# Kernel optimization log

Measured on AMD Instinct MI355X. Metric: run time of the kernel, lower is better.

The kernel has to match this reference:

```python
import jax, jax.numpy as jnp
import numpy as np

N_EXAMPLES = 10  # hardcoded repeat_interleave(10) in the source

def setup_inputs() -> dict:
    key = jax.random.key(0)
    k1, k2, k3, k4 = jax.random.split(key, 4)
    B, L, S, H = 8, 256, 512, 1024
    return {
        "output": jax.random.normal(k1, (B * N_EXAMPLES, L, H), dtype=jnp.float32),
        "context0": jax.random.normal(k2, (B * N_EXAMPLES, L, H), dtype=jnp.float32),
        "context1": jax.random.normal(k3, (B, S, H), dtype=jnp.float32),
        "mask": jnp.zeros((B * N_EXAMPLES, L), dtype=bool),
        "W_out": jax.random.normal(k4, (H, 3 * H), dtype=jnp.float32) * 0.02,
        "b_out": jnp.zeros((H,), dtype=jnp.float32),
    }

def reference(output, context0, context1, mask, W_out, b_out):
    # output, context0: [B*10, L, H]; context1: [B, S, H]
    # NOTE: in the torch source, `attn.data.masked_fill(mask, -inf)` is NOT
    # in-place and its result is discarded, so the mask has no effect on the
    # math. We reproduce that faithfully: `mask` is unused.
    del mask
    set_ctx = jnp.repeat(context1, N_EXAMPLES, axis=0)  # [B*10, S, H]
    # example-attention branch: bmm -> softmax -> bmm
    ex_attn = jax.nn.softmax(jnp.einsum('bld,bsd->bls', output, context0), axis=-1)  # [B*10, L, L]
    # set-attention branch: bmm -> softmax -> bmm
    set_attn = jax.nn.softmax(jnp.einsum('bld,bsd->bls', output, set_ctx), axis=-1)  # [B*10, L, S]
    ex_c = jnp.einsum('bls,bsd->bld', ex_attn, context0)   # [B*10, L, H]
    set_c = jnp.einsum('bls,bsd->bld', set_attn, set_ctx)  # [B*10, L, H]
    all_info = jnp.concatenate([output, ex_c, set_c], axis=-1)  # [B*10, L, 3H]
    out = jnp.tanh(jnp.einsum('blk,hk->blh', all_info, W_out) + b_out)  # [B*10, L, H]
    return (out, ex_attn, set_attn)
```

## Files before the change

kernel.cpp:

```cpp
#include <hip/hip_runtime.h>
#include <stdint.h>
#include <math.h>

typedef unsigned short u16;
typedef __attribute__((ext_vector_type(8))) short short8;
typedef __attribute__((ext_vector_type(4))) float floatx4;

__device__ __forceinline__ u16 f32_to_bf16(float f) {
    union { float f; uint32_t u; } v; v.f = f;
    uint32_t r = v.u + 0x7FFF + ((v.u >> 16) & 1);
    return (u16)(r >> 16);
}
__device__ __forceinline__ float bf16_to_f32(u16 h) {
    union { uint32_t u; float f; } v; v.u = ((uint32_t)h) << 16; return v.f;
}

__device__ __forceinline__ void gl_lds16(const u16* g, u16* l) {
    __builtin_amdgcn_global_load_lds(
        (const __attribute__((address_space(1))) void*)g,
        (__attribute__((address_space(3))) void*)l, 16, 0, 0);
}


__global__ void split_kernel(const float4* __restrict__ x, ushort4* __restrict__ hi,
                             ushort4* __restrict__ lo, long n4) {
    long i = (long)blockIdx.x * blockDim.x + threadIdx.x;
    if (i >= n4) return;
    float4 v = x[i];
    ushort4 h, l;
    h.x = f32_to_bf16(v.x); l.x = f32_to_bf16(v.x - bf16_to_f32(h.x));
    h.y = f32_to_bf16(v.y); l.y = f32_to_bf16(v.y - bf16_to_f32(h.y));
    h.z = f32_to_bf16(v.z); l.z = f32_to_bf16(v.z - bf16_to_f32(h.z));
    h.w = f32_to_bf16(v.w); l.w = f32_to_bf16(v.w - bf16_to_f32(h.w));
    hi[i] = h; lo[i] = l;
}

__global__ void conv_kernel(const float4* __restrict__ x, ushort4* __restrict__ hi, long n4) {
    long i = (long)blockIdx.x * blockDim.x + threadIdx.x;
    if (i >= n4) return;
    float4 v = x[i];
    ushort4 h;
    h.x = f32_to_bf16(v.x); h.y = f32_to_bf16(v.y);
    h.z = f32_to_bf16(v.z); h.w = f32_to_bf16(v.w);
    hi[i] = h;
}

__global__ void transpose_bf16(const float* __restrict__ src, u16* __restrict__ dst,
                               int R, int C) {
    __shared__ float tile[32][33];
    long base = (long)blockIdx.z * R * C;
    int c0 = blockIdx.x * 32, r0 = blockIdx.y * 32;
    #pragma unroll
    for (int i = threadIdx.y; i < 32; i += 8)
        tile[i][threadIdx.x] = src[base + (long)(r0 + i) * C + c0 + threadIdx.x];
    __syncthreads();
    #pragma unroll
    for (int i = threadIdx.y; i < 32; i += 8)
        dst[base + (long)(c0 + i) * R + r0 + threadIdx.x] = f32_to_bf16(tile[threadIdx.x][i]);
}

template <int VPT>
__global__ void softmax_rows(float* __restrict__ data, u16* __restrict__ outb) {
    const int SL = VPT * 64;
    int row = blockIdx.x * 4 + (threadIdx.x >> 6);
    int lane = threadIdx.x & 63;
    long base = (long)row * SL + lane;
    float v[VPT];
    #pragma unroll
    for (int i = 0; i < VPT; ++i) v[i] = data[base + i * 64];
    float m = v[0];
    #pragma unroll
    for (int i = 1; i < VPT; ++i) m = fmaxf(m, v[i]);
    #pragma unroll
    for (int off = 32; off > 0; off >>= 1) m = fmaxf(m, __shfl_xor(m, off, 64));
    float s = 0.f;
    #pragma unroll
    for (int i = 0; i < VPT; ++i) { v[i] = __expf(v[i] - m); s += v[i]; }
    #pragma unroll
    for (int off = 32; off > 0; off >>= 1) s += __shfl_xor(s, off, 64);
    float inv = 1.0f / s;
    #pragma unroll
    for (int i = 0; i < VPT; ++i) {
        float r = v[i] * inv;
        data[base + i * 64] = r;
        outb[base + i * 64] = f32_to_bf16(r);
    }
}

struct GemmP {
    const u16* A[3];
    const u16* B[3];
    long strideAb, strideBb, strideCb;
    int bdiv, nseg, Kper, lda, ldb, ldc, mode;
    float* Cf; u16* Cb; const float* bias;
};

__global__ __launch_bounds__(256) void gemm_bt(GemmP p) {
    __shared__ u16 As[128 * 64];
    __shared__ u16 Bs[128 * 64];
    const int tid  = threadIdx.x;
    const int lane = tid & 63;
    const int wave = tid >> 6;
    const int quad = lane >> 4;
    const int l15  = lane & 15;
    const int wm = (wave & 1) * 64;
    const int wn = (wave >> 1) * 64;
    const int m0 = blockIdx.x * 128;
    const int n0 = blockIdx.y * 128;
    const int bz = blockIdx.z;

    floatx4 acc[4][4];
    #pragma unroll
    for (int i = 0; i < 4; ++i)
        #pragma unroll
        for (int j = 0; j < 4; ++j)
            acc[i][j] = (floatx4){0.f, 0.f, 0.f, 0.f};

    const long aoff = (long)bz * p.strideAb;
    const long boff = (long)(bz / p.bdiv) * p.strideBb;

    for (int seg = 0; seg < p.nseg; ++seg) {
        const u16* Ag = p.A[seg] + aoff + (long)m0 * p.lda;
        const u16* Bg = p.B[seg] + boff + (long)n0 * p.ldb;
        for (int k0 = 0; k0 < p.Kper; k0 += 64) {
            __syncthreads();
            #pragma unroll
            for (int i = 0; i < 4; ++i) {
                const int flat = (i * 256 + tid) * 8;
                const int r = flat >> 6, c = flat & 63;
                gl_lds16(Ag + (long)r * p.lda + k0 + c, &As[flat]);
            }
            #pragma unroll
            for (int i = 0; i < 4; ++i) {
                const int flat = (i * 256 + tid) * 8;
                const int r = flat >> 6, c = flat & 63;
                gl_lds16(Bg + (long)r * p.ldb + k0 + c, &Bs[flat]);
            }
            __syncthreads();
            #pragma unroll
            for (int kk = 0; kk < 2; ++kk) {
                short8 af[4], bfr[4];
                #pragma unroll
                for (int i = 0; i < 4; ++i)
                    af[i] = *(const short8*)&As[(wm + i * 16 + l15) * 64 + kk * 32 + quad * 8];
                #pragma unroll
                for (int i = 0; i < 4; ++i)
                    bfr[i] = *(const short8*)&Bs[(wn + i * 16 + l15) * 64 + kk * 32 + quad * 8];
                #pragma unroll
                for (int mi = 0; mi < 4; ++mi)
                    #pragma unroll
                    for (int ni = 0; ni < 4; ++ni)
                        acc[mi][ni] = __builtin_amdgcn_mfma_f32_16x16x32_bf16(
                            af[mi], bfr[ni], acc[mi][ni], 0, 0, 0);
            }
        }
    }

    const long coff = (long)bz * p.strideCb;
    const int rb = m0 + wm + quad * 4;
    const int cbase = n0 + wn + l15;
    if (p.mode == 2) {
        #pragma unroll
        for (int ni = 0; ni < 4; ++ni) {
            const float bv = p.bias[cbase + ni * 16];
            #pragma unroll
            for (int mi = 0; mi < 4; ++mi)
                #pragma unroll
                for (int j = 0; j < 4; ++j)
                    p.Cf[coff + (long)(rb + mi * 16 + j) * p.ldc + cbase + ni * 16] =
                        tanhf(acc[mi][ni][j] + bv);
        }
    } else if (p.mode == 0) {
        #pragma unroll
        for (int ni = 0; ni < 4; ++ni)
            #pragma unroll
            for (int mi = 0; mi < 4; ++mi)
                #pragma unroll
                for (int j = 0; j < 4; ++j)
                    p.Cf[coff + (long)(rb + mi * 16 + j) * p.ldc + cbase + ni * 16] =
                        acc[mi][ni][j];
    } else {
        #pragma unroll
        for (int ni = 0; ni < 4; ++ni)
            #pragma unroll
            for (int mi = 0; mi < 4; ++mi)
                #pragma unroll
                for (int j = 0; j < 4; ++j)
                    p.Cb[coff + (long)(rb + mi * 16 + j) * p.ldc + cbase + ni * 16] =
                        f32_to_bf16(acc[mi][ni][j]);
    }
}

extern "C" void kernel_launch(void* const* d_in, const int* in_sizes, int n_in,
                              void* d_out, int out_size, void* d_ws, size_t ws_size,
                              hipStream_t stream) {
    const int BT = 80, L = 256, S = 512, H = 1024;
    const long NO   = (long)BT * L * H;
    const long NC1  = (long)8 * S * H;
    const long NW   = (long)H * 3 * H;
    const long NEXA = (long)BT * L * L;

    const float* X    = (const float*)d_in[0];
    const float* C0   = (const float*)d_in[1];
    const float* C1   = (const float*)d_in[2];
    const float* Wf   = (const float*)d_in[4];
    const float* bias = (const float*)d_in[5];

    float* out  = (float*)d_out;
    float* exa  = out + NO;
    float* seta = exa + NEXA;

    char* wsb = (char*)d_ws;
    size_t off = 0;
    auto alloc = [&](long nbytes) -> void* {
        void* p = (void*)(wsb + off);
        off += ((size_t)nbytes + 255) & ~(size_t)255;
        return p;
    };
    u16* Xhi  = (u16*)alloc(NO * 2);
    u16* Xlo  = (u16*)alloc(NO * 2);
    u16* C0hi = (u16*)alloc(NO * 2);
    u16* C0lo = (u16*)alloc(NO * 2);
    u16* C1hi = (u16*)alloc(NC1 * 2);
    u16* C1lo = (u16*)alloc(NC1 * 2);
    u16* Wb   = (u16*)alloc(NW * 2);
    u16* exab = (u16*)alloc(NEXA * 2);
    u16* setab= (u16*)alloc((long)BT * L * S * 2);
    u16* C0T = C0lo;
    u16* C1T = C1lo;
    u16* exc = Xlo;
    u16* setc = C0hi;

    split_kernel<<<(int)(NO / 4 / 256), 256, 0, stream>>>((const float4*)X, (ushort4*)Xhi, (ushort4*)Xlo, NO / 4);
    split_kernel<<<(int)(NO / 4 / 256), 256, 0, stream>>>((const float4*)C0, (ushort4*)C0hi, (ushort4*)C0lo, NO / 4);
    split_kernel<<<(int)(NC1 / 4 / 256), 256, 0, stream>>>((const float4*)C1, (ushort4*)C1hi, (ushort4*)C1lo, NC1 / 4);
    conv_kernel<<<(int)(NW / 4 / 256), 256, 0, stream>>>((const float4*)Wf, (ushort4*)Wb, NW / 4);

    {
        GemmP p{};
        p.A[0] = Xhi;  p.A[1] = Xlo;  p.A[2] = Xhi;
        p.B[0] = C0hi; p.B[1] = C0hi; p.B[2] = C0lo;
        p.strideAb = (long)L * H; p.strideBb = (long)L * H; p.strideCb = (long)L * L;
        p.bdiv = 1; p.nseg = 3; p.Kper = H; p.lda = H; p.ldb = H; p.ldc = L; p.mode = 0;
        p.Cf = exa; p.Cb = nullptr; p.bias = nullptr;
        gemm_bt<<<dim3(L / 128, L / 128, BT), 256, 0, stream>>>(p);
    }
    softmax_rows<4><<<BT * L / 4, 256, 0, stream>>>(exa, exab);

    {
        GemmP p{};
        p.A[0] = Xhi;  p.A[1] = Xlo;  p.A[2] = Xhi;
        p.B[0] = C1hi; p.B[1] = C1hi; p.B[2] = C1lo;
        p.strideAb = (long)L * H; p.strideBb = (long)S * H; p.strideCb = (long)L * S;
        p.bdiv = 10; p.nseg = 3; p.Kper = H; p.lda = H; p.ldb = H; p.ldc = S; p.mode = 0;
        p.Cf = seta; p.Cb = nullptr; p.bias = nullptr;
        gemm_bt<<<dim3(L / 128, S / 128, BT), 256, 0, stream>>>(p);
    }
    softmax_rows<8><<<BT * L / 4, 256, 0, stream>>>(seta, setab);

    transpose_bf16<<<dim3(H / 32, L / 32, BT), dim3(32, 8), 0, stream>>>(C0, C0T, L, H);
    transpose_bf16<<<dim3(H / 32, S / 32, 8), dim3(32, 8), 0, stream>>>(C1, C1T, S, H);

    {
        GemmP p{};
        p.A[0] = exab; p.A[1] = exab; p.A[2] = exab;
        p.B[0] = C0T;  p.B[1] = C0T;  p.B[2] = C0T;
        p.strideAb = (long)L * L; p.strideBb = (long)H * L; p.strideCb = (long)L * H;
        p.bdiv = 1; p.nseg = 1; p.Kper = L; p.lda = L; p.ldb = L; p.ldc = H; p.mode = 1;
        p.Cf = nullptr; p.Cb = exc; p.bias = nullptr;
        gemm_bt<<<dim3(L / 128, H / 128, BT), 256, 0, stream>>>(p);
    }
    {
        GemmP p{};
        p.A[0] = setab; p.A[1] = setab; p.A[2] = setab;
        p.B[0] = C1T;   p.B[1] = C1T;   p.B[2] = C1T;
        p.strideAb = (long)L * S; p.strideBb = (long)H * S; p.strideCb = (long)L * H;
        p.bdiv = 10; p.nseg = 1; p.Kper = S; p.lda = S; p.ldb = S; p.ldc = H; p.mode = 1;
        p.Cf = nullptr; p.Cb = setc; p.bias = nullptr;
        gemm_bt<<<dim3(L / 128, H / 128, BT), 256, 0, stream>>>(p);
    }
    {
        GemmP p{};
        p.A[0] = Xhi; p.A[1] = exc; p.A[2] = setc;
        p.B[0] = Wb;  p.B[1] = Wb + 1024; p.B[2] = Wb + 2048;
        p.strideAb = 0; p.strideBb = 0; p.strideCb = 0;
        p.bdiv = 1; p.nseg = 3; p.Kper = H; p.lda = H; p.ldb = 3 * H; p.ldc = H; p.mode = 2;
        p.Cf = out; p.Cb = nullptr; p.bias = bias;
        gemm_bt<<<dim3(BT * L / 128, H / 128, 1), 256, 0, stream>>>(p);
    }
}
```

Measured before the change: 911.4 us.

## XOR-swizzle GEMM LDS tiles and swap grid axes for N-major block order

Applies an XOR swizzle to the column chunk index when staging A/B tiles into shared memory and when reading them for MFMA, so the strided 64-element-row fragment reads no longer collide on the same LDS banks. The grid is also transposed so blockIdx.x walks the N dimension. Adjacent blocks then share the same A rows, which is meant to improve L2 reuse of the A tile. The risk is a mismatch between the swizzled write and read patterns, though the mapping looks consistent.

```diff
diff --git a/kernel.cpp b/kernel.cpp
--- a/kernel.cpp
+++ b/kernel.cpp
@@ -105,9 +105,13 @@
     const int l15  = lane & 15;
     const int wm = (wave & 1) * 64;
     const int wn = (wave >> 1) * 64;
-    const int m0 = blockIdx.x * 128;
-    const int n0 = blockIdx.y * 128;
+    const int n0 = blockIdx.x * 128;
+    const int m0 = blockIdx.y * 128;
     const int bz = blockIdx.z;
+
+    const int stg_r8 = tid >> 3;
+    const int stg_c  = ((tid & 7) ^ (stg_r8 & 7)) * 8;
+    const int xorl   = l15 & 7;
 
     floatx4 acc[4][4];
     #pragma unroll
@@ -126,26 +130,25 @@
             __syncthreads();
             #pragma unroll
             for (int i = 0; i < 4; ++i) {
-                const int flat = (i * 256 + tid) * 8;
-                const int r = flat >> 6, c = flat & 63;
-                gl_lds16(Ag + (long)r * p.lda + k0 + c, &As[flat]);
+                const int r = i * 32 + stg_r8;
+                gl_lds16(Ag + (long)r * p.lda + k0 + stg_c, &As[(i * 256 + tid) * 8]);
             }
             #pragma unroll
             for (int i = 0; i < 4; ++i) {
-                const int flat = (i * 256 + tid) * 8;
-                const int r = flat >> 6, c = flat & 63;
-                gl_lds16(Bg + (long)r * p.ldb + k0 + c, &Bs[flat]);
+                const int r = i * 32 + stg_r8;
+                gl_lds16(Bg + (long)r * p.ldb + k0 + stg_c, &Bs[(i * 256 + tid) * 8]);
             }
             __syncthreads();
             #pragma unroll
             for (int kk = 0; kk < 2; ++kk) {
+                const int cs = ((kk * 4 + quad) ^ xorl) * 8;
                 short8 af[4], bfr[4];
                 #pragma unroll
                 for (int i = 0; i < 4; ++i)
-                    af[i] = *(const short8*)&As[(wm + i * 16 + l15) * 64 + kk * 32 + quad * 8];
+                    af[i] = *(const short8*)&As[(wm + i * 16 + l15) * 64 + cs];
                 #pragma unroll
                 for (int i = 0; i < 4; ++i)
-                    bfr[i] = *(const short8*)&Bs[(wn + i * 16 + l15) * 64 + kk * 32 + quad * 8];
+                    bfr[i] = *(const short8*)&Bs[(wn + i * 16 + l15) * 64 + cs];
                 #pragma unroll
                 for (int mi = 0; mi < 4; ++mi)
                     #pragma unroll
@@ -254,7 +257,7 @@
         p.strideAb = (long)L * H; p.strideBb = (long)S * H; p.strideCb = (long)L * S;
         p.bdiv = 10; p.nseg = 3; p.Kper = H; p.lda = H; p.ldb = H; p.ldc = S; p.mode = 0;
         p.Cf = seta; p.Cb = nullptr; p.bias = nullptr;
-        gemm_bt<<<dim3(L / 128, S / 128, BT), 256, 0, stream>>>(p);
+        gemm_bt<<<dim3(S / 128, L / 128, BT), 256, 0, stream>>>(p);
     }
     softmax_rows<8><<<BT * L / 4, 256, 0, stream>>>(seta, setab);
 
@@ -268,7 +271,7 @@
         p.strideAb = (long)L * L; p.strideBb = (long)H * L; p.strideCb = (long)L * H;
         p.bdiv = 1; p.nseg = 1; p.Kper = L; p.lda = L; p.ldb = L; p.ldc = H; p.mode = 1;
         p.Cf = nullptr; p.Cb = exc; p.bias = nullptr;
-        gemm_bt<<<dim3(L / 128, H / 128, BT), 256, 0, stream>>>(p);
+        gemm_bt<<<dim3(H / 128, L / 128, BT), 256, 0, stream>>>(p);
     }
     {
         GemmP p{};
@@ -277,7 +280,7 @@
         p.strideAb = (long)L * S; p.strideBb = (long)H * S; p.strideCb = (long)L * H;
         p.bdiv = 10; p.nseg = 1; p.Kper = S; p.lda = S; p.ldb = S; p.ldc = H; p.mode = 1;
         p.Cf = nullptr; p.Cb = setc; p.bias = nullptr;
-        gemm_bt<<<dim3(L / 128, H / 128, BT), 256, 0, stream>>>(p);
+        gemm_bt<<<dim3(H / 128, L / 128, BT), 256, 0, stream>>>(p);
     }
     {
         GemmP p{};
@@ -286,6 +289,6 @@
         p.strideAb = 0; p.strideBb = 0; p.strideCb = 0;
         p.bdiv = 1; p.nseg = 3; p.Kper = H; p.lda = H; p.ldb = 3 * H; p.ldc = H; p.mode = 2;
         p.Cf = out; p.Cb = nullptr; p.bias = bias;
-        gemm_bt<<<dim3(BT * L / 128, H / 128, 1), 256, 0, stream>>>(p);
-    }
-}
+        gemm_bt<<<dim3(H / 128, BT * L / 128, 1), 256, 0, stream>>>(p);
+    }
+}
```

After: 847.3 us. 7.0% less time.
